# Kernel tuning notes

Measured on AMD Instinct MI355X. Metric: run time of the kernel, lower is better.

## Reference

```python
import jax, jax.numpy as jnp
import numpy as np

N_ATOMS = 10000
N_EDGES = 200000
L_MAX = 2
K_L = [32, 24, 16]  # k_max_l = n_element_channels * n_max_l

# (l1, l2, L) in the original loop order (l1 outer, l2 inner, L ascending)
PAIRS = [(0,0,0),(0,1,1),(0,2,2),
         (1,0,1),(1,1,0),(1,1,1),(1,1,2),(1,2,1),(1,2,2),
         (2,0,2),(2,1,1),(2,1,2),(2,2,0),(2,2,1),(2,2,2)]
# concatenated input width -> k_max_l[L] per (L, sigma) channel
LIN = {'0_1': (72, 32), '1_1': (80, 24), '1_m1': (40, 24), '2_1': (72, 16), '2_m1': (32, 16)}


def setup_inputs() -> dict:
    key = jax.random.key(0)
    it = iter(jax.random.split(key, 64))
    def nrm(shape):
        return jax.random.normal(next(it), shape, dtype=jnp.float32)
    inp = {}
    for l in range(L_MAX + 1):
        inp['rb%d' % l] = nrm((N_EDGES, K_L[l]))           # radial basis per l
    for l in range(L_MAX + 1):
        inp['sh%d' % l] = nrm((N_EDGES, 2*l+1, 1))         # spherical harmonics per l
    inp['emb'] = nrm((N_ATOMS, 1, K_L[0]))                 # initial center embedding
    for l in range(L_MAX + 1):
        inp['f%d' % l] = nrm((N_ATOMS, 2*l+1, K_L[l]))     # nu=1 equivariant features
    for (l1, l2, L) in PAIRS:
        inp['cg_%d_%d_%d' % (l1, l2, L)] = nrm(((2*l1+1)*(2*l2+1), 2*L+1))
    for LS, (fin, fout) in LIN.items():
        inp['W_' + LS] = nrm((fin, fout)) / np.float32(np.sqrt(fin))
        inp['b_' + LS] = nrm((fout,)) * 0.01
    inp['centers'] = jax.random.randint(next(it), (N_EDGES,), 0, N_ATOMS)
    inp['neighbors'] = jax.random.randint(next(it), (N_EDGES,), 0, N_ATOMS)
    inp['n_atoms'] = N_ATOMS
    return inp


def _normalize(x, dims):
    # Normalizer(dims): RMS normalization over the given dims
    return x * jax.lax.rsqrt(jnp.mean(x * x, axis=dims, keepdims=True) + 1e-12)


def _forward(floats, centers, neighbors, n_atoms):
    (rb0, rb1, rb2, sh0, sh1, sh2, emb, f0, f1, f2,
     cg_0_0_0, cg_0_1_1, cg_0_2_2, cg_1_0_1, cg_1_1_0, cg_1_1_1, cg_1_1_2,
     cg_1_2_1, cg_1_2_2, cg_2_0_2, cg_2_1_1, cg_2_1_2, cg_2_2_0, cg_2_2_1,
     cg_2_2_2, W_0_1, b_0_1, W_1_1, b_1_1, W_1_m1, b_1_m1, W_2_1, b_2_1,
     W_2_m1, b_2_m1) = floats
    rb = [rb0, rb1, rb2]; sh = [sh0, sh1, sh2]; feats = [f0, f1, f2]
    cgs = {'0_0_0': cg_0_0_0, '0_1_1': cg_0_1_1, '0_2_2': cg_0_2_2,
           '1_0_1': cg_1_0_1, '1_1_0': cg_1_1_0, '1_1_1': cg_1_1_1,
           '1_1_2': cg_1_1_2, '1_2_1': cg_1_2_1, '1_2_2': cg_1_2_2,
           '2_0_2': cg_2_0_2, '2_1_1': cg_2_1_1, '2_1_2': cg_2_1_2,
           '2_2_0': cg_2_2_0, '2_2_1': cg_2_2_1, '2_2_2': cg_2_2_2}
    lin = {'0_1': (W_0_1, b_0_1), '1_1': (W_1_1, b_1_1), '1_m1': (W_1_m1, b_1_m1),
           '2_1': (W_2_1, b_2_1), '2_m1': (W_2_m1, b_2_m1)}

    # ---- InvariantMessagePasser: density_l = scatter_add over centers of
    #      sh_l * rb_l * emb[neighbors]
    emb_n = emb[neighbors]                                       # [E, 1, k0]
    densities = []
    for l in range(L_MAX + 1):
        msg = sh[l] * rb[l][:, None, :] * emb_n[:, :, :K_L[l]]   # [E, 2l+1, k_l]
        densities.append(jax.ops.segment_sum(msg, centers, num_segments=n_atoms))

    # ---- EquivariantMessagePasser
    ve = [sh[l] * rb[l][:, None, :] for l in range(L_MAX + 1)]   # vector expansion [E,2l+1,k_l]
    fn = [feats[l][neighbors] for l in range(L_MAX + 1)]         # gathered neighbor feats
    results = {}
    for (l1, l2, L) in PAIRS:
        S = (-1) ** (l1 + l2 + L)
        k = min(K_L[l1], K_L[l2])
        t1 = ve[l1][:, :, :k]                                    # [E, 2l1+1, k]
        t2 = fn[l2][:, :, :k]                                    # [E, 2l2+1, k]
        cg = cgs['%d_%d_%d' % (l1, l2, L)].reshape(2*l1+1, 2*l2+1, 2*L+1)
        # fused outer product + CG contraction -> [E, 2L+1, k]
        res = jnp.einsum('eak,ebk,abM->eMk', t1, t2, cg)
        pooled = jax.ops.segment_sum(res, centers, num_segments=n_atoms)
        LS = '%d_%s' % (L, 'm1' if S < 0 else '1')
        results.setdefault(LS, []).append(pooled)

    outs = {}
    for LS, (W, b) in lin.items():
        x = jnp.concatenate(results[LS], axis=2)                 # [n_atoms, 2L+1, size_LS]
        x = _normalize(x, (0, 1))
        x = jnp.einsum('amf,fk->amk', x, W) + b
        outs[LS] = _normalize(x, (0, 1, 2))

    return (densities[0], densities[1], densities[2],
            outs['0_1'], outs['1_1'], outs['1_m1'], outs['2_1'], outs['2_m1'])


def reference(rb0, rb1, rb2, sh0, sh1, sh2, emb, f0, f1, f2,
              cg_0_0_0, cg_0_1_1, cg_0_2_2, cg_1_0_1, cg_1_1_0, cg_1_1_1,
              cg_1_1_2, cg_1_2_1, cg_1_2_2, cg_2_0_2, cg_2_1_1, cg_2_1_2,
              cg_2_2_0, cg_2_2_1, cg_2_2_2, W_0_1, b_0_1, W_1_1, b_1_1,
              W_1_m1, b_1_m1, W_2_1, b_2_1, W_2_m1, b_2_m1,
              centers, neighbors, n_atoms):
    floats = (rb0, rb1, rb2, sh0, sh1, sh2, emb, f0, f1, f2,
              cg_0_0_0, cg_0_1_1, cg_0_2_2, cg_1_0_1, cg_1_1_0, cg_1_1_1,
              cg_1_1_2, cg_1_2_1, cg_1_2_2, cg_2_0_2, cg_2_1_1, cg_2_1_2,
              cg_2_2_0, cg_2_2_1, cg_2_2_2, W_0_1, b_0_1, W_1_1, b_1_1,
              W_1_m1, b_1_m1, W_2_1, b_2_1, W_2_m1, b_2_m1)
    return _forward(floats, centers, neighbors, n_atoms)
```

## Files before the change

kernel.cpp:

```cpp
#include <hip/hip_runtime.h>
#include <hip/hip_bf16.h>

typedef __hip_bfloat16 bf16;

#define N_ATOMS 10000
#define N_EDGES 200000

#define SCG   0
#define SINV  616
#define SS1P  1024
#define SS2P  19968
#define SWS2  20288
#define SINTS 20352
#define IFLAG  0
#define ICOUNT 16
#define IOFFS  10016
#define ICURS  20032
#define IELIST 30032
#define INTS_END_SMALL 230032
#define INTS_END_BIG   430032
#define SXACC (SINTS + INTS_END_BIG)
#define BIG_FLOATS (SXACC + 952*N_ATOMS)

#define O0 0
#define O1 320000
#define O2 1040000
#define OY 1840000

__device__ __forceinline__ float b2f(bf16 x){ return __bfloat162float(x); }
__device__ __forceinline__ bf16  f2b(float x){ return __float2bfloat16(x); }

__device__ __forceinline__ float ldv(const float* p, int i){ return p[i]; }
__device__ __forceinline__ float ldv(const bf16*  p, int i){ return b2f(p[i]); }
__device__ __forceinline__ void  stv(float* p, int i, float v){ p[i] = v; }
__device__ __forceinline__ void  stv(bf16*  p, int i, float v){ p[i] = f2b(v); }

template<typename T> __device__ __forceinline__ int dtid();
// ... 85 lines not shown
    elist[offs[c] + p] = e;
  }
}

__global__ void k_scatter2(const int* __restrict__ centers, const int* __restrict__ neighbors,
                           const int* __restrict__ offs, int* __restrict__ cursors,
                           int2* __restrict__ elist2) {
  int e = blockIdx.x*blockDim.x + threadIdx.x;
  if (e < N_EDGES) {
    int c = centers[e];
    int p = atomicAdd(&cursors[c], 1);
    elist2[offs[c] + p] = make_int2(e, neighbors[e]);
  }
}

template<typename T, int MODE>
__global__ __launch_bounds__(256) void k_main(
    const T* __restrict__ rb0, const T* __restrict__ rb1, const T* __restrict__ rb2,
    const T* __restrict__ sh0, const T* __restrict__ sh1, const T* __restrict__ sh2,
    const T* __restrict__ emb, const T* __restrict__ f0, const T* __restrict__ f1,
    const T* __restrict__ f2, const int* __restrict__ neighbors,
    const int* __restrict__ offs, const int* __restrict__ elist,
    const float* __restrict__ cgf, float* __restrict__ s1p,
    const float* __restrict__ inv, float* __restrict__ s2p,
    float* __restrict__ xout, LinP lp, T* __restrict__ out,
    const int* __restrict__ flag)
{
  if (flag[0] != dtid<T>()) return;
  int lane = threadIdx.x & 63;
  int wv   = threadIdx.x >> 6;
  int a = blockIdx.x;
  int beg = offs[a];
  int cnt = offs[a+1] - beg;
  int k32 = lane & 31, e2 = lane >> 5;
  int k16 = lane & 15, e4 = lane >> 4;
  const int2* el2 = (const int2*)elist;
  int ab = a & 63;

  __shared__ float L[952];
  __shared__ float red[4][5];

  float acc[20];
  #pragma unroll
  for (int i = 0; i < 20; ++i) acc[i] = 0.f;

  if (wv == 0) {
    const float* C000 = cgf + 0;
    const float* C011 = cgf + 1;
    const float* C101 = cgf + 35;
    const float* C110 = cgf + 44;
    const float* C111 = cgf + 53;
    const float* C112 = cgf + 80;
    for (int base = 0; base < cnt; base += 2) {
      int idx = base + e2;
      if (idx < cnt) {
        int e, n;
        if constexpr (MODE == 0) { int2 en = el2[beg + idx]; e = en.x; n = en.y; }
        else { e = elist[beg + idx]; n = neighbors[e]; }
        float s0 = ldv(sh0, e);
        float s1a0 = ldv(sh1, e*3+0), s1a1 = ldv(sh1, e*3+1), s1a2 = ldv(sh1, e*3+2);
        float rb0k = ldv(rb0, e*32 + k32);
        float ek   = ldv(emb, n*32 + k32);
        float f0k  = ldv(f0,  n*32 + k32);
        float ve0 = s0 * rb0k;
        acc[0] = fmaf(ve0, ek, acc[0]);
        acc[4] = fmaf(C000[0]*ve0, f0k, acc[4]);
        if (k32 < 24) {
          float rb1k = ldv(rb1, e*24 + k32);
          float f1k0 = ldv(f1, n*72 + k32);
          float f1k1 = ldv(f1, n*72 + 24 + k32);
          float f1k2 = ldv(f1, n*72 + 48 + k32);
          float rbek = rb1k * ek;
          acc[1] = fmaf(s1a0, rbek, acc[1]);
// ... 29 lines not shown
              for (int M = 0; M < 5; ++M) acc[15+M] = fmaf(p, C112[q*5+M], acc[15+M]);
            }
          }
        }
      }
    }
    #pragma unroll
    for (int i = 0; i < 20; ++i) acc[i] += __shfl_xor(acc[i], 32);
  } else if (wv == 1) {
    const float* C022 = cgf + 10;
    const float* C121 = cgf + 125;
    const float* C122 = cgf + 170;
    for (int base = 0; base < cnt; base += 4) {
      int idx = base + e4;
      if (idx < cnt) {
        int e, n;
        if constexpr (MODE == 0) { int2 en = el2[beg + idx]; e = en.x; n = en.y; }
        else { e = elist[beg + idx]; n = neighbors[e]; }
        float s0 = ldv(sh0, e);
        float s1a[3];
        #pragma unroll
        for (int m = 0; m < 3; ++m) s1a[m] = ldv(sh1, e*3+m);
        float s2a[5];
        #pragma unroll
        for (int m = 0; m < 5; ++m) s2a[m] = ldv(sh2, e*5+m);
        float rb0k = ldv(rb0, e*32 + k16);
        float rb1k = ldv(rb1, e*24 + k16);
        float rb2k = ldv(rb2, e*16 + k16);
        float ek   = ldv(emb, n*32 + k16);
        float f2k[5];
        #pragma unroll
        for (int b = 0; b < 5; ++b) f2k[b] = ldv(f2, n*80 + b*16 + k16);
        float re = rb2k * ek;
// ... 21 lines not shown
        }
      }
    }
    #pragma unroll
    for (int i = 0; i < 18; ++i) {
      acc[i] += __shfl_xor(acc[i], 16);
      acc[i] += __shfl_xor(acc[i], 32);
    }
  } else if (wv == 2) {
    const float* C202 = cgf + 245;
    const float* C211 = cgf + 270;
    const float* C212 = cgf + 315;
    for (int base = 0; base < cnt; base += 4) {
      int idx = base + e4;
      if (idx < cnt) {
        int e, n;
        if constexpr (MODE == 0) { int2 en = el2[beg + idx]; e = en.x; n = en.y; }
        else { e = elist[beg + idx]; n = neighbors[e]; }
        float s2a[5];
        #pragma unroll
        for (int m = 0; m < 5; ++m) s2a[m] = ldv(sh2, e*5+m);
        float rb2k = ldv(rb2, e*16 + k16);
        float f0k  = ldv(f0,  n*32 + k16);
        float f1k[3];
        #pragma unroll
        for (int b = 0; b < 3; ++b) f1k[b] = ldv(f1, n*72 + b*24 + k16);
        float g9 = rb2k * f0k;
        #pragma unroll
        for (int aa = 0; aa < 5; ++aa) {
          float p = g9 * s2a[aa];
          #pragma unroll
          for (int M = 0; M < 5; ++M) acc[0+M] = fmaf(p, C202[aa*5+M], acc[0+M]);
        }
// ... 12 lines not shown
        }
      }
    }
    #pragma unroll
    for (int i = 0; i < 13; ++i) {
      acc[i] += __shfl_xor(acc[i], 16);
      acc[i] += __shfl_xor(acc[i], 32);
    }
  } else {
    const float* C220 = cgf + 390;
    const float* C221 = cgf + 415;
    const float* C222 = cgf + 490;
    for (int base = 0; base < cnt; base += 4) {
      int idx = base + e4;
      if (idx < cnt) {
        int e, n;
        if constexpr (MODE == 0) { int2 en = el2[beg + idx]; e = en.x; n = en.y; }
        else { e = elist[beg + idx]; n = neighbors[e]; }
        float s2a[5];
        #pragma unroll
        for (int m = 0; m < 5; ++m) s2a[m] = ldv(sh2, e*5+m);
        float rb2k = ldv(rb2, e*16 + k16);
        float f2k[5];
        #pragma unroll
        for (int b = 0; b < 5; ++b) f2k[b] = ldv(f2, n*80 + b*16 + k16);
        #pragma unroll
        for (int aa = 0; aa < 5; ++aa) {
          float sa = rb2k * s2a[aa];
          #pragma unroll
          for (int bb = 0; bb < 5; ++bb) {
            float p = sa * f2k[bb];
            int q = aa*5+bb;
            acc[0] = fmaf(p, C220[q], acc[0]);
            #pragma unroll
            for (int M = 0; M < 3; ++M) acc[1+M] = fmaf(p, C221[q*3+M], acc[1+M]);
            #pragma unroll
            for (int M = 0; M < 5; ++M) acc[4+M] = fmaf(p, C222[q*5+M], acc[4+M]);
          }
        }
      }
    }
    #pragma unroll
    for (int i = 0; i < 9; ++i) {
      acc[i] += __shfl_xor(acc[i], 16);
      acc[i] += __shfl_xor(acc[i], 32);
    }
  }

  if constexpr (MODE != 2) {
    if (wv == 0) {
      if (lane < 32) {
        stv(out, O0 + a*32 + k32, acc[0]);
        atomicAdd(&s1p[(0+k32)*64+ab], acc[4]*acc[4]);
        if (k32 < 24) {
          #pragma unroll
          for (int m = 0; m < 3; ++m) stv(out, O1 + a*72 + m*24 + k32, acc[1+m]);
          atomicAdd(&s1p[(32+k32)*64+ab], acc[11]*acc[11]);
          float q;
          q = acc[5]*acc[5]+acc[6]*acc[6]+acc[7]*acc[7];
          atomicAdd(&s1p[(72+k32)*64+ab], q);
          q = acc[8]*acc[8]+acc[9]*acc[9]+acc[10]*acc[10];
          atomicAdd(&s1p[(96+k32)*64+ab], q);
          q = acc[12]*acc[12]+acc[13]*acc[13]+acc[14]*acc[14];
          atomicAdd(&s1p[(152+k32)*64+ab], q);
          q = acc[15]*acc[15]+acc[16]*acc[16]+acc[17]*acc[17]
            + acc[18]*acc[18]+acc[19]*acc[19];
          atomicAdd(&s1p[(208+k32)*64+ab], q);
        }
      }
    } else if (wv == 1) {
      if (lane < 16) {
        #pragma unroll
        for (int m = 0; m < 5; ++m) stv(out, O2 + a*80 + m*16 + k16, acc[m]);
        float q;
        q = acc[5]*acc[5]+acc[6]*acc[6]+acc[7]*acc[7]+acc[8]*acc[8]+acc[9]*acc[9];
        atomicAdd(&s1p[(192+k16)*64+ab], q);
        q = acc[10]*acc[10]+acc[11]*acc[11]+acc[12]*acc[12];
        atomicAdd(&s1p[(120+k16)*64+ab], q);
        q = acc[13]*acc[13]+acc[14]*acc[14]+acc[15]*acc[15]
          + acc[16]*acc[16]+acc[17]*acc[17];
        atomicAdd(&s1p[(264+k16)*64+ab], q);
      }
    } else if (wv == 2) {
      if (lane < 16) {
        float q;
        q = acc[0]*acc[0]+acc[1]*acc[1]+acc[2]*acc[2]+acc[3]*acc[3]+acc[4]*acc[4];
        atomicAdd(&s1p[(232+k16)*64+ab], q);
        q = acc[5]*acc[5]+acc[6]*acc[6]+acc[7]*acc[7];
        atomicAdd(&s1p[(136+k16)*64+ab], q);
        q = acc[8]*acc[8]+acc[9]*acc[9]+acc[10]*acc[10]
          + acc[11]*acc[11]+acc[12]*acc[12];
        atomicAdd(&s1p[(280+k16)*64+ab], q);
      }
    } else {
      if (lane < 16) {
        atomicAdd(&s1p[(56+k16)*64+ab], acc[0]*acc[0]);
        float q;
        q = acc[1]*acc[1]+acc[2]*acc[2]+acc[3]*acc[3];
        atomicAdd(&s1p[(176+k16)*64+ab], q);
        q = acc[4]*acc[4]+acc[5]*acc[5]+acc[6]*acc[6]
          + acc[7]*acc[7]+acc[8]*acc[8];
        atomicAdd(&s1p[(248+k16)*64+ab], q);
      }
    }
  }

  if constexpr (MODE == 0) {
    float* xg = xout + a*952;
    if (wv == 0) {
      if (lane < 32) {
        xg[k32] = acc[4];
        if (k32 < 24) {
          xg[32+k32] = acc[11];
          #pragma unroll
          for (int M = 0; M < 3; ++M) xg[72+M*80+k32]     = acc[5+M];
          #pragma unroll
          for (int M = 0; M < 3; ++M) xg[72+M*80+24+k32]  = acc[8+M];
          #pragma unroll
          for (int M = 0; M < 3; ++M) xg[312+M*40+k32]    = acc[12+M];
          #pragma unroll
          for (int M = 0; M < 5; ++M) xg[432+M*72+16+k32] = acc[15+M];
        }
      }
    } else if (wv == 1) {
      if (lane < 16) {
        #pragma unroll
        for (int M = 0; M < 5; ++M) xg[432+M*72+k16]    = acc[5+M];
        #pragma unroll
        for (int M = 0; M < 3; ++M) xg[72+M*80+48+k16]  = acc[10+M];
        #pragma unroll
        for (int M = 0; M < 5; ++M) xg[792+M*32+k16]    = acc[13+M];
      }
    } else if (wv == 2) {
      if (lane < 16) {
        #pragma unroll
        for (int M = 0; M < 5; ++M) xg[432+M*72+40+k16] = acc[0+M];
        #pragma unroll
        for (int M = 0; M < 3; ++M) xg[72+M*80+64+k16]  = acc[5+M];
        #pragma unroll
        for (int M = 0; M < 5; ++M) xg[792+M*32+16+k16] = acc[8+M];
      }
    } else {
      if (lane < 16) {
        xg[56+k16] = acc[0];
        #pragma unroll
        for (int M = 0; M < 3; ++M) xg[312+M*40+24+k16] = acc[1+M];
        #pragma unroll
        for (int M = 0; M < 5; ++M) xg[432+M*72+56+k16] = acc[4+M];
      }
    }
  }

  if constexpr (MODE == 2) {
    if (wv == 0) {
      if (lane < 32) {
        L[k32] = acc[4]*inv[k32];
        if (k32 < 24) {
          L[32+k32] = acc[11]*inv[32+k32];
          #pragma unroll
          for (int M = 0; M < 3; ++M) L[72+M*80+k32]     = acc[5+M]*inv[72+k32];
          #pragma unroll
          for (int M = 0; M < 3; ++M) L[72+M*80+24+k32]  = acc[8+M]*inv[96+k32];
          #pragma unroll
          for (int M = 0; M < 3; ++M) L[312+M*40+k32]    = acc[12+M]*inv[152+k32];
          #pragma unroll
          for (int M = 0; M < 5; ++M) L[432+M*72+16+k32] = acc[15+M]*inv[208+k32];
        }
      }
    } else if (wv == 1) {
      if (lane < 16) {
        #pragma unroll
        for (int M = 0; M < 5; ++M) L[432+M*72+k16]    = acc[5+M]*inv[192+k16];
        #pragma unroll
        for (int M = 0; M < 3; ++M) L[72+M*80+48+k16]  = acc[10+M]*inv[120+k16];
        #pragma unroll
        for (int M = 0; M < 5; ++M) L[792+M*32+k16]    = acc[13+M]*inv[264+k16];
      }
    } else if (wv == 2) {
      if (lane < 16) {
        #pragma unroll
        for (int M = 0; M < 5; ++M) L[432+M*72+40+k16] = acc[0+M]*inv[232+k16];
        #pragma unroll
        for (int M = 0; M < 3; ++M) L[72+M*80+64+k16]  = acc[5+M]*inv[136+k16];
        #pragma unroll
        for (int M = 0; M < 5; ++M) L[792+M*32+16+k16] = acc[8+M]*inv[280+k16];
      }
    } else {
      if (lane < 16) {
        L[56+k16] = acc[0]*inv[56+k16];
        #pragma unroll
        for (int M = 0; M < 3; ++M) L[312+M*40+24+k16] = acc[1+M]*inv[176+k16];
        #pragma unroll
        for (int M = 0; M < 5; ++M) L[432+M*72+56+k16] = acc[4+M]*inv[248+k16];
      }
    }
    __syncthreads();
    int t = threadIdx.x;
    float y2[5] = {0.f,0.f,0.f,0.f,0.f};
    for (int tau = t; tau < 336; tau += 256) {
      int ls = 0;
      while (tau >= c_cum[ls+1]) ++ls;
      int rem = tau - c_cum[ls];
      int kn = c_kout[ls], fin = c_fin[ls];
      int M = rem / kn, ko = rem - M*kn;
      const T* W = (const T*)lp.W[ls];
      float y = ldv((const T*)lp.B[ls], ko);
      const float* xv = &L[c_xb[ls] + M*fin];
      for (int f = 0; f < fin; ++f) y = fmaf(xv[f], ldv(W, f*kn+ko), y);
      stv(out, c_yoff[ls] + (a*c_Ms[ls] + M)*kn + ko, y);
      y2[ls] += y*y;
    }
    #pragma unroll
    for (int i = 0; i < 5; ++i) {
      y2[i] += __shfl_xor(y2[i], 1);  y2[i] += __shfl_xor(y2[i], 2);
      y2[i] += __shfl_xor(y2[i], 4);  y2[i] += __shfl_xor(y2[i], 8);
      y2[i] += __shfl_xor(y2[i], 16); y2[i] += __shfl_xor(y2[i], 32);
    }
    if (lane == 0) {
      #pragma unroll
      for (int i = 0; i < 5; ++i) red[wv][i] = y2[i];
    }
    __syncthreads();
    if (t == 0) {
      #pragma unroll
      for (int i = 0; i < 5; ++i)
        atomicAdd(&s2p[i*64 + ab], red[0][i]+red[1][i]+red[2][i]+red[3][i]);
    }
  }
}

template<typename T>
__global__ __launch_bounds__(256) void k_lin(
    const float* __restrict__ xg, const float* __restrict__ inv,
    LinP lp, T* __restrict__ out, float* __restrict__ s2p,
    const int* __restrict__ flag)
{
  if (flag[0] != dtid<T>()) return;
  int a = blockIdx.x;
  int t = threadIdx.x;
  __shared__ float L[952];
  for (int i = t; i < 952; i += 256) {
    int ch;
    if      (i < 72)  ch = i;
    else if (i < 312) ch = 72  + (i-72)  % 80;
    else if (i < 432) ch = 152 + (i-312) % 40;
    else if (i < 792) ch = 192 + (i-432) % 72;
    else              ch = 264 + (i-792) % 32;
    L[i] = xg[a*952 + i] * inv[ch];
  }
  __syncthreads();
  float y2[5] = {0.f,0.f,0.f,0.f,0.f};
  for (int tau = t; tau < 336; tau += 256) {
    int ls = 0;
    while (tau >= c_cum[ls+1]) ++ls;
    int rem = tau - c_cum[ls];
    int kn = c_kout[ls], fin = c_fin[ls];
    int M = rem / kn, ko = rem - M*kn;
    const T* W = (const T*)lp.W[ls];
    float y = ldv((const T*)lp.B[ls], ko);
    const float* xv = &L[c_xb[ls] + M*fin];
    for (int f = 0; f < fin; ++f) y = fmaf(xv[f], ldv(W, f*kn+ko), y);
    stv(out, c_yoff[ls] + (a*c_Ms[ls] + M)*kn + ko, y);
    y2[ls] += y*y;
// ... 37 lines not shown
}

template<typename T>
__global__ void k_scale(const float* __restrict__ ws2, T* __restrict__ out,
                        const int* __restrict__ flag) {
  if (flag[0] != dtid<T>()) return;
  int i = blockIdx.x*blockDim.x + threadIdx.x;
  if (i >= 3360000) return;
  int ls = (i < 320000) ? 0 : (i < 1040000) ? 1 : (i < 1760000) ? 2 : (i < 2560000) ? 3 : 4;
  float scale = rsqrtf(ws2[ls] / (float)c_numel[ls] + 1e-12f);
  stv(out, OY + i, ldv((const T*)out, OY + i) * scale);
}

template<typename T>
static void launch_chain(void* const* d_in, T* out, float* wsf, int* wsi,
                         Ptrs15 cg, LinP lp, bool big, hipStream_t stream) {
  const T* rb0 = (const T*)d_in[0];
  const T* rb1 = (const T*)d_in[1];
  const T* rb2 = (const T*)d_in[2];
  const T* sh0 = (const T*)d_in[3];
  const T* sh1 = (const T*)d_in[4];
  const T* sh2 = (const T*)d_in[5];
  const T* emb = (const T*)d_in[6];
  const T* f0  = (const T*)d_in[7];
  const T* f1  = (const T*)d_in[8];
  const T* f2  = (const T*)d_in[9];
  const int* neighbors = (const int*)d_in[36];
  const int* flag = wsi + IFLAG;

  k_cg<T><<<3, 256, 0, stream>>>(cg, wsf, flag);
  if (big) {
    k_main<T,0><<<N_ATOMS, 256, 0, stream>>>(rb0, rb1, rb2, sh0, sh1, sh2, emb, f0, f1, f2,
        neighbors, wsi+IOFFS, wsi+IELIST, wsf+SCG, wsf+SS1P, nullptr, nullptr,
        wsf+SXACC, lp, out, flag);
    k_red1<<<296, 64, 0, stream>>>(wsf+SS1P, wsf+SINV);
    k_lin<T><<<N_ATOMS, 256, 0, stream>>>(wsf+SXACC, wsf+SINV, lp, out, wsf+SS2P, flag);
  } else {
    k_main<T,1><<<N_ATOMS, 256, 0, stream>>>(rb0, rb1, rb2, sh0, sh1, sh2, emb, f0, f1, f2,
        neighbors, wsi+IOFFS, wsi+IELIST, wsf+SCG, wsf+SS1P, nullptr, nullptr,
        nullptr, lp, out, flag);
    k_red1<<<296, 64, 0, stream>>>(wsf+SS1P, wsf+SINV);
    k_main<T,2><<<N_ATOMS, 256, 0, stream>>>(rb0, rb1, rb2, sh0, sh1, sh2, emb, f0, f1, f2,
        neighbors, wsi+IOFFS, wsi+IELIST, wsf+SCG, nullptr, wsf+SINV, wsf+SS2P,
        nullptr, lp, out, flag);
  }
  k_red2<<<5, 64, 0, stream>>>(wsf+SS2P, wsf+SWS2);
  k_scale<T><<<(3360000+255)/256, 256, 0, stream>>>(wsf+SWS2, out, flag);
}

extern "C" void kernel_launch(void* const* d_in, const int* in_sizes, int n_in,
                              void* d_out, int out_size, void* d_ws, size_t ws_size,
                              hipStream_t stream) {
  float* wsf = (float*)d_ws;
  int*   wsi = (int*)(wsf + SINTS);
  const int* centers   = (const int*)d_in[35];
  const int* neighbors = (const int*)d_in[36];
  bool big = ws_size >= (size_t)BIG_FLOATS * 4;

  Ptrs15 cg;
  for (int i = 0; i < 15; ++i) cg.p[i] = d_in[10+i];
  LinP lp;
  lp.W[0] = d_in[25]; lp.B[0] = d_in[26];
  lp.W[1] = d_in[27]; lp.B[1] = d_in[28];
  lp.W[2] = d_in[29]; lp.B[2] = d_in[30];
  lp.W[3] = d_in[31]; lp.B[3] = d_in[32];
  lp.W[4] = d_in[33]; lp.B[4] = d_in[34];

  k_probe<<<1, 64, 0, stream>>>((const unsigned short*)d_in[0],
                                (const unsigned short*)d_in[6], wsi + IFLAG);
  k_zero<<<154, 256, 0, stream>>>(wsf, wsi);
  k_hist<<<(N_EDGES+255)/256, 256, 0, stream>>>(centers, wsi+ICOUNT);
  k_scan<<<1, 1024, 0, stream>>>(wsi+ICOUNT, wsi+IOFFS);
  if (big) {
    k_scatter2<<<(N_EDGES+255)/256, 256, 0, stream>>>(centers, neighbors, wsi+IOFFS,
                                                      wsi+ICURS, (int2*)(wsi+IELIST));
  } else {
    k_scatter<<<(N_EDGES+255)/256, 256, 0, stream>>>(centers, wsi+IOFFS, wsi+ICURS, wsi+IELIST);
  }

  launch_chain<bf16 >(d_in, (bf16*)d_out,  wsf, wsi, cg, lp, big, stream);
  launch_chain<float>(d_in, (float*)d_out, wsf, wsi, cg, lp, big, stream);
}
```

Measured before the change: 516.4 us.

## Split per-atom edge kernel into 13 balanced single-wave work groups

Replaces the 4-wave-per-atom main kernel, whose waves carried very unequal numbers of CG products, with a kernel that launches 13 single-wave blocks per atom. Each block handles a smaller, more even subset of the tensor-product outputs. The pre-linear intermediate buffer is now stored in bf16 instead of fp32, which cuts its write and read traffic. In exchange, neighbor features and edge data are re-gathered by several groups per atom, and the intermediate loses precision.

```diff
diff --git a/kernel.cpp b/kernel.cpp
--- a/kernel.cpp
+++ b/kernel.cpp
@@ -5,6 +5,7 @@
 
 #define N_ATOMS 10000
 #define N_EDGES 200000
+#define NGRP 13
 
 #define SCG   0
 #define SINV  616
@@ -19,8 +20,8 @@
 #define IELIST 30032
 #define INTS_END_SMALL 230032
 #define INTS_END_BIG   430032
-#define SXACC (SINTS + INTS_END_BIG)
-#define BIG_FLOATS (SXACC + 952*N_ATOMS)
+#define XBF_BYTE_OFF ((size_t)SINTS*4 + (size_t)INTS_END_BIG*4)
+#define BIG_BYTES (XBF_BYTE_OFF + (size_t)952*N_ATOMS*2)
 
 #define O0 0
 #define O1 320000
@@ -136,16 +137,381 @@
   }
 }
 
-template<typename T, int MODE>
-__global__ __launch_bounds__(256) void k_main(
+template<typename T, int BIGX>
+__global__ __launch_bounds__(64) void k_grp(
     const T* __restrict__ rb0, const T* __restrict__ rb1, const T* __restrict__ rb2,
     const T* __restrict__ sh0, const T* __restrict__ sh1, const T* __restrict__ sh2,
     const T* __restrict__ emb, const T* __restrict__ f0, const T* __restrict__ f1,
     const T* __restrict__ f2, const int* __restrict__ neighbors,
     const int* __restrict__ offs, const int* __restrict__ elist,
     const float* __restrict__ cgf, float* __restrict__ s1p,
-    const float* __restrict__ inv, float* __restrict__ s2p,
-    float* __restrict__ xout, LinP lp, T* __restrict__ out,
+    bf16* __restrict__ xout, T* __restrict__ out, const int* __restrict__ flag)
+{
+  if (flag[0] != dtid<T>()) return;
+  int bx = blockIdx.x;
+  int g = bx % NGRP, a = bx / NGRP;
+  int lane = threadIdx.x;
+  int beg = offs[a];
+  int cnt = offs[a+1] - beg;
+  int k32 = lane & 31, e2 = lane >> 5;
+  int k16 = lane & 15, e4 = lane >> 4;
+  int ab = a & 63;
+  const int2* el2 = (const int2*)elist;
+  bf16* xg = xout + a*952;
+
+#define FETCH_EN(idx) int e, n; \
+    if constexpr (BIGX) { int2 en = el2[beg + (idx)]; e = en.x; n = en.y; } \
+    else { e = elist[beg + (idx)]; n = neighbors[e]; }
+
+  if (g == 0) {
+    const float* C011 = cgf + 1;
+    const float* C101 = cgf + 35;
+    const float* C110 = cgf + 44;
+    float C000v = cgf[0];
+    float acc[12];
+    #pragma unroll
+    for (int i = 0; i < 12; ++i) acc[i] = 0.f;
+    for (int base = 0; base < cnt; base += 2) {
+      int idx = base + e2;
+      if (idx < cnt) {
+        FETCH_EN(idx)
+        float s0 = ldv(sh0, e);
+        float s1a0 = ldv(sh1, e*3+0), s1a1 = ldv(sh1, e*3+1), s1a2 = ldv(sh1, e*3+2);
+        float rb0k = ldv(rb0, e*32 + k32);
+        float ek   = ldv(emb, n*32 + k32);
+        float f0k  = ldv(f0,  n*32 + k32);
+        float ve0 = s0 * rb0k;
+        acc[0] = fmaf(ve0, ek, acc[0]);
+        acc[4] = fmaf(C000v*ve0, f0k, acc[4]);
+        if (k32 < 24) {
+          float rb1k = ldv(rb1, e*24 + k32);
+          float f1k0 = ldv(f1, n*72 + k32);
+          float f1k1 = ldv(f1, n*72 + 24 + k32);
+          float f1k2 = ldv(f1, n*72 + 48 + k32);
+          float rbek = rb1k * ek;
+          acc[1] = fmaf(s1a0, rbek, acc[1]);
+          acc[2] = fmaf(s1a1, rbek, acc[2]);
+          acc[3] = fmaf(s1a2, rbek, acc[3]);
+          #pragma unroll
+          for (int bb = 0; bb < 3; ++bb) {
+            float fb = (bb==0)?f1k0:(bb==1)?f1k1:f1k2;
+            float p = ve0 * fb;
+            #pragma unroll
+            for (int M = 0; M < 3; ++M) acc[5+M] = fmaf(p, C011[bb*3+M], acc[5+M]);
+          }
+          float gv = rb1k * f0k;
+          #pragma unroll
+          for (int aa = 0; aa < 3; ++aa) {
+            float sa = (aa==0)?s1a0:(aa==1)?s1a1:s1a2;
+            float p = gv * sa;
+            #pragma unroll
+            for (int M = 0; M < 3; ++M) acc[8+M] = fmaf(p, C101[aa*3+M], acc[8+M]);
+          }
+          #pragma unroll
+          for (int aa = 0; aa < 3; ++aa) {
+            float sa = rb1k * ((aa==0)?s1a0:(aa==1)?s1a1:s1a2);
+            #pragma unroll
+            for (int bb = 0; bb < 3; ++bb) {
+              float fb = (bb==0)?f1k0:(bb==1)?f1k1:f1k2;
+              acc[11] = fmaf(sa*fb, C110[aa*3+bb], acc[11]);
+            }
+          }
+        }
+      }
+    }
+    #pragma unroll
+    for (int i = 0; i < 12; ++i) acc[i] += __shfl_xor(acc[i], 32);
+    if (lane < 32) {
+      stv(out, O0 + a*32 + k32, acc[0]);
+      atomicAdd(&s1p[(0+k32)*64+ab], acc[4]*acc[4]);
+      if (BIGX) xg[k32] = f2b(acc[4]);
+      if (k32 < 24) {
+        #pragma unroll
+        for (int m = 0; m < 3; ++m) stv(out, O1 + a*72 + m*24 + k32, acc[1+m]);
+        atomicAdd(&s1p[(32+k32)*64+ab], acc[11]*acc[11]);
+        atomicAdd(&s1p[(72+k32)*64+ab], acc[5]*acc[5]+acc[6]*acc[6]+acc[7]*acc[7]);
+        atomicAdd(&s1p[(96+k32)*64+ab], acc[8]*acc[8]+acc[9]*acc[9]+acc[10]*acc[10]);
+        if (BIGX) {
+          xg[32+k32] = f2b(acc[11]);
+          #pragma unroll
+          for (int M = 0; M < 3; ++M) xg[72+M*80+k32]    = f2b(acc[5+M]);
+          #pragma unroll
+          for (int M = 0; M < 3; ++M) xg[72+M*80+24+k32] = f2b(acc[8+M]);
+        }
+      }
+    }
+  } else if (g == 1 || g == 2) {
+    const float* C = (g == 1) ? (cgf + 53) : (cgf + 80);
+    const int NM = (g == 1) ? 3 : 5;
+    float acc[5] = {0.f,0.f,0.f,0.f,0.f};
+    for (int base = 0; base < cnt; base += 2) {
+      int idx = base + e2;
+      if (idx < cnt && k32 < 24) {
+        FETCH_EN(idx)
+        float s1a0 = ldv(sh1, e*3+0), s1a1 = ldv(sh1, e*3+1), s1a2 = ldv(sh1, e*3+2);
+        float rb1k = ldv(rb1, e*24 + k32);
+        float f1k0 = ldv(f1, n*72 + k32);
+        float f1k1 = ldv(f1, n*72 + 24 + k32);
+        float f1k2 = ldv(f1, n*72 + 48 + k32);
+        #pragma unroll
+        for (int aa = 0; aa < 3; ++aa) {
+          float sa = rb1k * ((aa==0)?s1a0:(aa==1)?s1a1:s1a2);
+          #pragma unroll
+          for (int bb = 0; bb < 3; ++bb) {
+            float fb = (bb==0)?f1k0:(bb==1)?f1k1:f1k2;
+            float p = sa * fb;
+            int q = aa*3+bb;
+            for (int M = 0; M < NM; ++M) acc[M] = fmaf(p, C[q*NM+M], acc[M]);
+          }
+        }
+      }
+    }
+    #pragma unroll
+    for (int i = 0; i < 5; ++i) acc[i] += __shfl_xor(acc[i], 32);
+    if (lane < 24) {
+      float q2 = 0.f;
+      for (int M = 0; M < NM; ++M) q2 += acc[M]*acc[M];
+      int ch = (g == 1) ? (152+k32) : (208+k32);
+      atomicAdd(&s1p[ch*64+ab], q2);
+      if (BIGX) {
+        if (g == 1) { for (int M = 0; M < 3; ++M) xg[312+M*40+k32]    = f2b(acc[M]); }
+        else        { for (int M = 0; M < 5; ++M) xg[432+M*72+16+k32] = f2b(acc[M]); }
+      }
+    }
+  } else if (g == 3) {
+    const float* C022 = cgf + 10;
+    float acc[10];
+    #pragma unroll
+    for (int i = 0; i < 10; ++i) acc[i] = 0.f;
+    for (int base = 0; base < cnt; base += 4) {
+      int idx = base + e4;
+      if (idx < cnt) {
+        FETCH_EN(idx)
+        float s2a[5];
+        #pragma unroll
+        for (int m = 0; m < 5; ++m) s2a[m] = ldv(sh2, e*5+m);
+        float rb2k = ldv(rb2, e*16 + k16);
+        float ek   = ldv(emb, n*32 + k16);
+        float re = rb2k * ek;
+        #pragma unroll
+        for (int m = 0; m < 5; ++m) acc[m] = fmaf(s2a[m], re, acc[m]);
+        float s0 = ldv(sh0, e);
+        float rb0k = ldv(rb0, e*32 + k16);
+        float ve0 = s0 * rb0k;
+        #pragma unroll
+        for (int bb = 0; bb < 5; ++bb) {
+          float p = ve0 * ldv(f2, n*80 + bb*16 + k16);
+          #pragma unroll
+          for (int M = 0; M < 5; ++M) acc[5+M] = fmaf(p, C022[bb*5+M], acc[5+M]);
+        }
+      }
+    }
+    #pragma unroll
+    for (int i = 0; i < 10; ++i) {
+      acc[i] += __shfl_xor(acc[i], 16);
+      acc[i] += __shfl_xor(acc[i], 32);
+    }
+    if (lane < 16) {
+      #pragma unroll
+      for (int m = 0; m < 5; ++m) stv(out, O2 + a*80 + m*16 + k16, acc[m]);
+      atomicAdd(&s1p[(192+k16)*64+ab],
+                acc[5]*acc[5]+acc[6]*acc[6]+acc[7]*acc[7]+acc[8]*acc[8]+acc[9]*acc[9]);
+      if (BIGX) { for (int M = 0; M < 5; ++M) xg[432+M*72+k16] = f2b(acc[5+M]); }
+    }
+  } else if (g == 4 || g == 5) {
+    const float* C = (g == 4) ? (cgf + 125) : (cgf + 170);
+    const int NM = (g == 4) ? 3 : 5;
+    float acc[5] = {0.f,0.f,0.f,0.f,0.f};
+    for (int base = 0; base < cnt; base += 4) {
+      int idx = base + e4;
+      if (idx < cnt) {
+        FETCH_EN(idx)
+        float s1a[3];
+        #pragma unroll
+        for (int m = 0; m < 3; ++m) s1a[m] = ldv(sh1, e*3+m);
+        float rb1k = ldv(rb1, e*24 + k16);
+        float f2k[5];
+        #pragma unroll
+        for (int b = 0; b < 5; ++b) f2k[b] = ldv(f2, n*80 + b*16 + k16);
+        #pragma unroll
+        for (int aa = 0; aa < 3; ++aa) {
+          float sa = rb1k * s1a[aa];
+          #pragma unroll
+          for (int bb = 0; bb < 5; ++bb) {
+            float p = sa * f2k[bb];
+            int q = aa*5+bb;
+            for (int M = 0; M < NM; ++M) acc[M] = fmaf(p, C[q*NM+M], acc[M]);
+          }
+        }
+      }
+    }
+    #pragma unroll
+    for (int i = 0; i < 5; ++i) {
+      acc[i] += __shfl_xor(acc[i], 16);
+      acc[i] += __shfl_xor(acc[i], 32);
+    }
+    if (lane < 16) {
+      float q2 = 0.f;
+      for (int M = 0; M < NM; ++M) q2 += acc[M]*acc[M];
+      int ch = (g == 4) ? (120+k16) : (264+k16);
+      atomicAdd(&s1p[ch*64+ab], q2);
+      if (BIGX) {
+        if (g == 4) { for (int M = 0; M < 3; ++M) xg[72+M*80+48+k16] = f2b(acc[M]); }
+        else        { for (int M = 0; M < 5; ++M) xg[792+M*32+k16]   = f2b(acc[M]); }
+      }
+    }
+  } else if (g == 6) {
+    const float* C202 = cgf + 245;
+    float acc[5] = {0.f,0.f,0.f,0.f,0.f};
+    for (int base = 0; base < cnt; base += 4) {
+      int idx = base + e4;
+      if (idx < cnt) {
+        FETCH_EN(idx)
+        float s2a[5];
+        #pragma unroll
+        for (int m = 0; m < 5; ++m) s2a[m] = ldv(sh2, e*5+m);
+        float rb2k = ldv(rb2, e*16 + k16);
+        float f0k  = ldv(f0,  n*32 + k16);
+        float gv = rb2k * f0k;
+        #pragma unroll
+        for (int aa = 0; aa < 5; ++aa) {
+          float p = gv * s2a[aa];
+          #pragma unroll
+          for (int M = 0; M < 5; ++M) acc[M] = fmaf(p, C202[aa*5+M], acc[M]);
+        }
+      }
+    }
+    #pragma unroll
+    for (int i = 0; i < 5; ++i) {
+      acc[i] += __shfl_xor(acc[i], 16);
+      acc[i] += __shfl_xor(acc[i], 32);
+    }
+    if (lane < 16) {
+      atomicAdd(&s1p[(232+k16)*64+ab],
+                acc[0]*acc[0]+acc[1]*acc[1]+acc[2]*acc[2]+acc[3]*acc[3]+acc[4]*acc[4]);
+      if (BIGX) { for (int M = 0; M < 5; ++M) xg[432+M*72+40+k16] = f2b(acc[M]); }
+    }
+  } else if (g == 7 || g == 8) {
+    const float* C = (g == 7) ? (cgf + 270) : (cgf + 315);
+    const int NM = (g == 7) ? 3 : 5;
+    float acc[5] = {0.f,0.f,0.f,0.f,0.f};
+    for (int base = 0; base < cnt; base += 4) {
+      int idx = base + e4;
+      if (idx < cnt) {
+        FETCH_EN(idx)
+        float s2a[5];
+        #pragma unroll
+        for (int m = 0; m < 5; ++m) s2a[m] = ldv(sh2, e*5+m);
+        float rb2k = ldv(rb2, e*16 + k16);
+        float f1k[3];
+        #pragma unroll
+        for (int b = 0; b < 3; ++b) f1k[b] = ldv(f1, n*72 + b*24 + k16);
+        #pragma unroll
+        for (int aa = 0; aa < 5; ++aa) {
+          float sa = rb2k * s2a[aa];
+          #pragma unroll
+          for (int bb = 0; bb < 3; ++bb) {
+            float p = sa * f1k[bb];
+            int q = aa*3+bb;
+            for (int M = 0; M < NM; ++M) acc[M] = fmaf(p, C[q*NM+M], acc[M]);
+          }
+        }
+      }
+    }
+    #pragma unroll
+    for (int i = 0; i < 5; ++i) {
+      acc[i] += __shfl_xor(acc[i], 16);
+      acc[i] += __shfl_xor(acc[i], 32);
+    }
+    if (lane < 16) {
+      float q2 = 0.f;
+      for (int M = 0; M < NM; ++M) q2 += acc[M]*acc[M];
+      int ch = (g == 7) ? (136+k16) : (280+k16);
+      atomicAdd(&s1p[ch*64+ab], q2);
+      if (BIGX) {
+        if (g == 7) { for (int M = 0; M < 3; ++M) xg[72+M*80+64+k16]  = f2b(acc[M]); }
+        else        { for (int M = 0; M < 5; ++M) xg[792+M*32+16+k16] = f2b(acc[M]); }
+      }
+    }
+  } else {
+    const float* C220 = cgf + 390;
+    const float* C221 = cgf + 415;
+    const float* C222 = cgf + 490;
+    float acc[3] = {0.f,0.f,0.f};
+    for (int base = 0; base < cnt; base += 4) {
+      int idx = base + e4;
+      if (idx < cnt) {
+        FETCH_EN(idx)
+        float s2a[5];
+        #pragma unroll
+        for (int m = 0; m < 5; ++m) s2a[m] = ldv(sh2, e*5+m);
+        float rb2k = ldv(rb2, e*16 + k16);
+        float f2k[5];
+        #pragma unroll
+        for (int b = 0; b < 5; ++b) f2k[b] = ldv(f2, n*80 + b*16 + k16);
+        #pragma unroll
+        for (int aa = 0; aa < 5; ++aa) {
+          float sa = rb2k * s2a[aa];
+          #pragma unroll
+          for (int bb = 0; bb < 5; ++bb) {
+            float p = sa * f2k[bb];
+            int q = aa*5+bb;
+            if (g == 9) {
+              acc[0] = fmaf(p, C220[q],     acc[0]);
+              acc[1] = fmaf(p, C221[q*3],   acc[1]);
+            } else if (g == 10) {
+              acc[0] = fmaf(p, C221[q*3+1], acc[0]);
+              acc[1] = fmaf(p, C221[q*3+2], acc[1]);
+            } else if (g == 11) {
+              acc[0] = fmaf(p, C222[q*5],   acc[0]);
+              acc[1] = fmaf(p, C222[q*5+1], acc[1]);
+            } else {
+              acc[0] = fmaf(p, C222[q*5+2], acc[0]);
+              acc[1] = fmaf(p, C222[q*5+3], acc[1]);
+              acc[2] = fmaf(p, C222[q*5+4], acc[2]);
+            }
+          }
+        }
+      }
+    }
+    #pragma unroll
+    for (int i = 0; i < 3; ++i) {
+      acc[i] += __shfl_xor(acc[i], 16);
+      acc[i] += __shfl_xor(acc[i], 32);
+    }
+    if (lane < 16) {
+      if (g == 9) {
+        atomicAdd(&s1p[(56+k16)*64+ab],  acc[0]*acc[0]);
+        atomicAdd(&s1p[(176+k16)*64+ab], acc[1]*acc[1]);
+        if (BIGX) { xg[56+k16] = f2b(acc[0]); xg[312+24+k16] = f2b(acc[1]); }
+      } else if (g == 10) {
+        atomicAdd(&s1p[(176+k16)*64+ab], acc[0]*acc[0]+acc[1]*acc[1]);
+        if (BIGX) { xg[312+40+24+k16] = f2b(acc[0]); xg[312+80+24+k16] = f2b(acc[1]); }
+      } else if (g == 11) {
+        atomicAdd(&s1p[(248+k16)*64+ab], acc[0]*acc[0]+acc[1]*acc[1]);
+        if (BIGX) { xg[432+56+k16] = f2b(acc[0]); xg[432+72+56+k16] = f2b(acc[1]); }
+      } else {
+        atomicAdd(&s1p[(248+k16)*64+ab],
+                  acc[0]*acc[0]+acc[1]*acc[1]+acc[2]*acc[2]);
+        if (BIGX) {
+          #pragma unroll
+          for (int j = 0; j < 3; ++j) xg[432+(2+j)*72+56+k16] = f2b(acc[j]);
+        }
+      }
+    }
+  }
+#undef FETCH_EN
+}
+
+template<typename T>
+__global__ __launch_bounds__(256) void k_pass2(
+    const T* __restrict__ rb0, const T* __restrict__ rb1, const T* __restrict__ rb2,
+    const T* __restrict__ sh0, const T* __restrict__ sh1, const T* __restrict__ sh2,
+    const T* __restrict__ emb, const T* __restrict__ f0, const T* __restrict__ f1,
+    const T* __restrict__ f2, const int* __restrict__ neighbors,
+    const int* __restrict__ offs, const int* __restrict__ elist,
+    const float* __restrict__ cgf, const float* __restrict__ inv,
+    float* __restrict__ s2p, LinP lp, T* __restrict__ out,
     const int* __restrict__ flag)
 {
   if (flag[0] != dtid<T>()) return;
@@ -156,7 +522,6 @@
   int cnt = offs[a+1] - beg;
   int k32 = lane & 31, e2 = lane >> 5;
   int k16 = lane & 15, e4 = lane >> 4;
-  const int2* el2 = (const int2*)elist;
   int ab = a & 63;
 
   __shared__ float L[952];
@@ -176,9 +541,8 @@
     for (int base = 0; base < cnt; base += 2) {
       int idx = base + e2;
       if (idx < cnt) {
-        int e, n;
-        if constexpr (MODE == 0) { int2 en = el2[beg + idx]; e = en.x; n = en.y; }
-        else { e = elist[beg + idx]; n = neighbors[e]; }
+        int e = elist[beg + idx];
+        int n = neighbors[e];
         float s0 = ldv(sh0, e);
         float s1a0 = ldv(sh1, e*3+0), s1a1 = ldv(sh1, e*3+1), s1a2 = ldv(sh1, e*3+2);
         float rb0k = ldv(rb0, e*32 + k32);
@@ -238,9 +602,8 @@
     for (int base = 0; base < cnt; base += 4) {
       int idx = base + e4;
       if (idx < cnt) {
-        int e, n;
-        if constexpr (MODE == 0) { int2 en = el2[beg + idx]; e = en.x; n = en.y; }
-        else { e = elist[beg + idx]; n = neighbors[e]; }
+        int e = elist[beg + idx];
+        int n = neighbors[e];
         float s0 = ldv(sh0, e);
         float s1a[3];
         #pragma unroll
@@ -292,9 +655,8 @@
     for (int base = 0; base < cnt; base += 4) {
       int idx = base + e4;
       if (idx < cnt) {
-        int e, n;
-        if constexpr (MODE == 0) { int2 en = el2[beg + idx]; e = en.x; n = en.y; }
-        else { e = elist[beg + idx]; n = neighbors[e]; }
+        int e = elist[beg + idx];
+        int n = neighbors[e];
         float s2a[5];
         #pragma unroll
         for (int m = 0; m < 5; ++m) s2a[m] = ldv(sh2, e*5+m);
@@ -337,9 +699,8 @@
     for (int base = 0; base < cnt; base += 4) {
       int idx = base + e4;
       if (idx < cnt) {
-        int e, n;
-        if constexpr (MODE == 0) { int2 en = el2[beg + idx]; e = en.x; n = en.y; }
-        else { e = elist[beg + idx]; n = neighbors[e]; }
+        int e = elist[beg + idx];
+        int n = neighbors[e];
         float s2a[5];
         #pragma unroll
         for (int m = 0; m < 5; ++m) s2a[m] = ldv(sh2, e*5+m);
@@ -370,191 +731,85 @@
     }
   }
 
-  if constexpr (MODE != 2) {
-    if (wv == 0) {
-      if (lane < 32) {
-        stv(out, O0 + a*32 + k32, acc[0]);
-        atomicAdd(&s1p[(0+k32)*64+ab], acc[4]*acc[4]);
-        if (k32 < 24) {
-          #pragma unroll
-          for (int m = 0; m < 3; ++m) stv(out, O1 + a*72 + m*24 + k32, acc[1+m]);
-          atomicAdd(&s1p[(32+k32)*64+ab], acc[11]*acc[11]);
-          float q;
-          q = acc[5]*acc[5]+acc[6]*acc[6]+acc[7]*acc[7];
-          atomicAdd(&s1p[(72+k32)*64+ab], q);
-          q = acc[8]*acc[8]+acc[9]*acc[9]+acc[10]*acc[10];
-          atomicAdd(&s1p[(96+k32)*64+ab], q);
-          q = acc[12]*acc[12]+acc[13]*acc[13]+acc[14]*acc[14];
-          atomicAdd(&s1p[(152+k32)*64+ab], q);
-          q = acc[15]*acc[15]+acc[16]*acc[16]+acc[17]*acc[17]
-            + acc[18]*acc[18]+acc[19]*acc[19];
-          atomicAdd(&s1p[(208+k32)*64+ab], q);
-        }
-      }
-    } else if (wv == 1) {
-      if (lane < 16) {
-        #pragma unroll
-        for (int m = 0; m < 5; ++m) stv(out, O2 + a*80 + m*16 + k16, acc[m]);
-        float q;
-        q = acc[5]*acc[5]+acc[6]*acc[6]+acc[7]*acc[7]+acc[8]*acc[8]+acc[9]*acc[9];
-        atomicAdd(&s1p[(192+k16)*64+ab], q);
-        q = acc[10]*acc[10]+acc[11]*acc[11]+acc[12]*acc[12];
-        atomicAdd(&s1p[(120+k16)*64+ab], q);
-        q = acc[13]*acc[13]+acc[14]*acc[14]+acc[15]*acc[15]
-          + acc[16]*acc[16]+acc[17]*acc[17];
-        atomicAdd(&s1p[(264+k16)*64+ab], q);
-      }
-    } else if (wv == 2) {
-      if (lane < 16) {
-        float q;
-        q = acc[0]*acc[0]+acc[1]*acc[1]+acc[2]*acc[2]+acc[3]*acc[3]+acc[4]*acc[4];
-        atomicAdd(&s1p[(232+k16)*64+ab], q);
-        q = acc[5]*acc[5]+acc[6]*acc[6]+acc[7]*acc[7];
-        atomicAdd(&s1p[(136+k16)*64+ab], q);
-        q = acc[8]*acc[8]+acc[9]*acc[9]+acc[10]*acc[10]
-          + acc[11]*acc[11]+acc[12]*acc[12];
-        atomicAdd(&s1p[(280+k16)*64+ab], q);
-      }
-    } else {
-      if (lane < 16) {
-        atomicAdd(&s1p[(56+k16)*64+ab], acc[0]*acc[0]);
-        float q;
-        q = acc[1]*acc[1]+acc[2]*acc[2]+acc[3]*acc[3];
-        atomicAdd(&s1p[(176+k16)*64+ab], q);
-        q = acc[4]*acc[4]+acc[5]*acc[5]+acc[6]*acc[6]
-          + acc[7]*acc[7]+acc[8]*acc[8];
-        atomicAdd(&s1p[(248+k16)*64+ab], q);
-      }
-    }
-  }
-
-  if constexpr (MODE == 0) {
-    float* xg = xout + a*952;
-    if (wv == 0) {
-      if (lane < 32) {
-        xg[k32] = acc[4];
-        if (k32 < 24) {
-          xg[32+k32] = acc[11];
-          #pragma unroll
-          for (int M = 0; M < 3; ++M) xg[72+M*80+k32]     = acc[5+M];
-          #pragma unroll
-          for (int M = 0; M < 3; ++M) xg[72+M*80+24+k32]  = acc[8+M];
-          #pragma unroll
-          for (int M = 0; M < 3; ++M) xg[312+M*40+k32]    = acc[12+M];
-          #pragma unroll
-          for (int M = 0; M < 5; ++M) xg[432+M*72+16+k32] = acc[15+M];
-        }
-      }
-    } else if (wv == 1) {
-      if (lane < 16) {
-        #pragma unroll
-        for (int M = 0; M < 5; ++M) xg[432+M*72+k16]    = acc[5+M];
-        #pragma unroll
-        for (int M = 0; M < 3; ++M) xg[72+M*80+48+k16]  = acc[10+M];
-        #pragma unroll
-        for (int M = 0; M < 5; ++M) xg[792+M*32+k16]    = acc[13+M];
-      }
-    } else if (wv == 2) {
-      if (lane < 16) {
-        #pragma unroll
-        for (int M = 0; M < 5; ++M) xg[432+M*72+40+k16] = acc[0+M];
-        #pragma unroll
-        for (int M = 0; M < 3; ++M) xg[72+M*80+64+k16]  = acc[5+M];
-        #pragma unroll
-        for (int M = 0; M < 5; ++M) xg[792+M*32+16+k16] = acc[8+M];
-      }
-    } else {
-      if (lane < 16) {
-        xg[56+k16] = acc[0];
-        #pragma unroll
-        for (int M = 0; M < 3; ++M) xg[312+M*40+24+k16] = acc[1+M];
-        #pragma unroll
-        for (int M = 0; M < 5; ++M) xg[432+M*72+56+k16] = acc[4+M];
-      }
-    }
-  }
-
-  if constexpr (MODE == 2) {
-    if (wv == 0) {
-      if (lane < 32) {
-        L[k32] = acc[4]*inv[k32];
-        if (k32 < 24) {
-          L[32+k32] = acc[11]*inv[32+k32];
-          #pragma unroll
-          for (int M = 0; M < 3; ++M) L[72+M*80+k32]     = acc[5+M]*inv[72+k32];
-          #pragma unroll
-          for (int M = 0; M < 3; ++M) L[72+M*80+24+k32]  = acc[8+M]*inv[96+k32];
-          #pragma unroll
-          for (int M = 0; M < 3; ++M) L[312+M*40+k32]    = acc[12+M]*inv[152+k32];
-          #pragma unroll
-          for (int M = 0; M < 5; ++M) L[432+M*72+16+k32] = acc[15+M]*inv[208+k32];
-        }
-      }
-    } else if (wv == 1) {
-      if (lane < 16) {
-        #pragma unroll
-        for (int M = 0; M < 5; ++M) L[432+M*72+k16]    = acc[5+M]*inv[192+k16];
-        #pragma unroll
-        for (int M = 0; M < 3; ++M) L[72+M*80+48+k16]  = acc[10+M]*inv[120+k16];
-        #pragma unroll
-        for (int M = 0; M < 5; ++M) L[792+M*32+k16]    = acc[13+M]*inv[264+k16];
-      }
-    } else if (wv == 2) {
-      if (lane < 16) {
-        #pragma unroll
-        for (int M = 0; M < 5; ++M) L[432+M*72+40+k16] = acc[0+M]*inv[232+k16];
-        #pragma unroll
-        for (int M = 0; M < 3; ++M) L[72+M*80+64+k16]  = acc[5+M]*inv[136+k16];
-        #pragma unroll
-        for (int M = 0; M < 5; ++M) L[792+M*32+16+k16] = acc[8+M]*inv[280+k16];
-      }
-    } else {
-      if (lane < 16) {
-        L[56+k16] = acc[0]*inv[56+k16];
-        #pragma unroll
-        for (int M = 0; M < 3; ++M) L[312+M*40+24+k16] = acc[1+M]*inv[176+k16];
-        #pragma unroll
-        for (int M = 0; M < 5; ++M) L[432+M*72+56+k16] = acc[4+M]*inv[248+k16];
-      }
-    }
-    __syncthreads();
-    int t = threadIdx.x;
-    float y2[5] = {0.f,0.f,0.f,0.f,0.f};
-    for (int tau = t; tau < 336; tau += 256) {
-      int ls = 0;
-      while (tau >= c_cum[ls+1]) ++ls;
-      int rem = tau - c_cum[ls];
-      int kn = c_kout[ls], fin = c_fin[ls];
-      int M = rem / kn, ko = rem - M*kn;
-      const T* W = (const T*)lp.W[ls];
-      float y = ldv((const T*)lp.B[ls], ko);
-      const float* xv = &L[c_xb[ls] + M*fin];
-      for (int f = 0; f < fin; ++f) y = fmaf(xv[f], ldv(W, f*kn+ko), y);
-      stv(out, c_yoff[ls] + (a*c_Ms[ls] + M)*kn + ko, y);
-      y2[ls] += y*y;
-    }
-    #pragma unroll
-    for (int i = 0; i < 5; ++i) {
-      y2[i] += __shfl_xor(y2[i], 1);  y2[i] += __shfl_xor(y2[i], 2);
-      y2[i] += __shfl_xor(y2[i], 4);  y2[i] += __shfl_xor(y2[i], 8);
-      y2[i] += __shfl_xor(y2[i], 16); y2[i] += __shfl_xor(y2[i], 32);
-    }
-    if (lane == 0) {
+  if (wv == 0) {
+    if (lane < 32) {
+      L[k32] = acc[4]*inv[k32];
+      if (k32 < 24) {
+        L[32+k32] = acc[11]*inv[32+k32];
+        #pragma unroll
+        for (int M = 0; M < 3; ++M) L[72+M*80+k32]     = acc[5+M]*inv[72+k32];
+        #pragma unroll
+        for (int M = 0; M < 3; ++M) L[72+M*80+24+k32]  = acc[8+M]*inv[96+k32];
+        #pragma unroll
+        for (int M = 0; M < 3; ++M) L[312+M*40+k32]    = acc[12+M]*inv[152+k32];
+        #pragma unroll
+        for (int M = 0; M < 5; ++M) L[432+M*72+16+k32] = acc[15+M]*inv[208+k32];
+      }
+    }
+  } else if (wv == 1) {
+    if (lane < 16) {
       #pragma unroll
-      for (int i = 0; i < 5; ++i) red[wv][i] = y2[i];
-    }
-    __syncthreads();
-    if (t == 0) {
+      for (int M = 0; M < 5; ++M) L[432+M*72+k16]    = acc[5+M]*inv[192+k16];
       #pragma unroll
-      for (int i = 0; i < 5; ++i)
-        atomicAdd(&s2p[i*64 + ab], red[0][i]+red[1][i]+red[2][i]+red[3][i]);
-    }
+      for (int M = 0; M < 3; ++M) L[72+M*80+48+k16]  = acc[10+M]*inv[120+k16];
+      #pragma unroll
+      for (int M = 0; M < 5; ++M) L[792+M*32+k16]    = acc[13+M]*inv[264+k16];
+    }
+  } else if (wv == 2) {
+    if (lane < 16) {
+      #pragma unroll
+      for (int M = 0; M < 5; ++M) L[432+M*72+40+k16] = acc[0+M]*inv[232+k16];
+      #pragma unroll
+      for (int M = 0; M < 3; ++M) L[72+M*80+64+k16]  = acc[5+M]*inv[136+k16];
+      #pragma unroll
+      for (int M = 0; M < 5; ++M) L[792+M*32+16+k16] = acc[8+M]*inv[280+k16];
+    }
+  } else {
+    if (lane < 16) {
+      L[56+k16] = acc[0]*inv[56+k16];
+      #pragma unroll
+      for (int M = 0; M < 3; ++M) L[312+M*40+24+k16] = acc[1+M]*inv[176+k16];
+      #pragma unroll
+      for (int M = 0; M < 5; ++M) L[432+M*72+56+k16] = acc[4+M]*inv[248+k16];
+    }
+  }
+  __syncthreads();
+  int t = threadIdx.x;
+  float y2[5] = {0.f,0.f,0.f,0.f,0.f};
+  for (int tau = t; tau < 336; tau += 256) {
+    int ls = 0;
+    while (tau >= c_cum[ls+1]) ++ls;
+    int rem = tau - c_cum[ls];
+    int kn = c_kout[ls], fin = c_fin[ls];
+    int M = rem / kn, ko = rem - M*kn;
+    const T* W = (const T*)lp.W[ls];
+    float y = ldv((const T*)lp.B[ls], ko);
+    const float* xv = &L[c_xb[ls] + M*fin];
+    for (int f = 0; f < fin; ++f) y = fmaf(xv[f], ldv(W, f*kn+ko), y);
+    stv(out, c_yoff[ls] + (a*c_Ms[ls] + M)*kn + ko, y);
+    y2[ls] += y*y;
+  }
+  #pragma unroll
+  for (int i = 0; i < 5; ++i) {
+    y2[i] += __shfl_xor(y2[i], 1);  y2[i] += __shfl_xor(y2[i], 2);
+    y2[i] += __shfl_xor(y2[i], 4);  y2[i] += __shfl_xor(y2[i], 8);
+    y2[i] += __shfl_xor(y2[i], 16); y2[i] += __shfl_xor(y2[i], 32);
+  }
+  if (lane == 0) {
+    #pragma unroll
+    for (int i = 0; i < 5; ++i) red[wv][i] = y2[i];
+  }
+  __syncthreads();
+  if (t == 0) {
+    #pragma unroll
+    for (int i = 0; i < 5; ++i)
+      atomicAdd(&s2p[i*64 + ab], red[0][i]+red[1][i]+red[2][i]+red[3][i]);
   }
 }
 
 template<typename T>
 __global__ __launch_bounds__(256) void k_lin(
-    const float* __restrict__ xg, const float* __restrict__ inv,
+    const bf16* __restrict__ xg, const float* __restrict__ inv,
     LinP lp, T* __restrict__ out, float* __restrict__ s2p,
     const int* __restrict__ flag)
 {
@@ -569,7 +824,7 @@
     else if (i < 432) ch = 152 + (i-312) % 40;
     else if (i < 792) ch = 192 + (i-432) % 72;
     else              ch = 264 + (i-792) % 32;
-    L[i] = xg[a*952 + i] * inv[ch];
+    L[i] = b2f(xg[a*952 + i]) * inv[ch];
   }
   __syncthreads();
   float y2[5] = {0.f,0.f,0.f,0.f,0.f};
@@ -637,7 +892,8 @@
 
 template<typename T>
 static void launch_chain(void* const* d_in, T* out, float* wsf, int* wsi,
-                         Ptrs15 cg, LinP lp, bool big, hipStream_t stream) {
+                         bf16* xbf, Ptrs15 cg, LinP lp, bool big,
+                         hipStream_t stream) {
   const T* rb0 = (const T*)d_in[0];
   const T* rb1 = (const T*)d_in[1];
   const T* rb2 = (const T*)d_in[2];
@@ -653,19 +909,19 @@
 
   k_cg<T><<<3, 256, 0, stream>>>(cg, wsf, flag);
   if (big) {
-    k_main<T,0><<<N_ATOMS, 256, 0, stream>>>(rb0, rb1, rb2, sh0, sh1, sh2, emb, f0, f1, f2,
-        neighbors, wsi+IOFFS, wsi+IELIST, wsf+SCG, wsf+SS1P, nullptr, nullptr,
-        wsf+SXACC, lp, out, flag);
+    k_grp<T,1><<<N_ATOMS*NGRP, 64, 0, stream>>>(rb0, rb1, rb2, sh0, sh1, sh2, emb,
+        f0, f1, f2, neighbors, wsi+IOFFS, wsi+IELIST, wsf+SCG, wsf+SS1P,
+        xbf, out, flag);
     k_red1<<<296, 64, 0, stream>>>(wsf+SS1P, wsf+SINV);
-    k_lin<T><<<N_ATOMS, 256, 0, stream>>>(wsf+SXACC, wsf+SINV, lp, out, wsf+SS2P, flag);
+    k_lin<T><<<N_ATOMS, 256, 0, stream>>>(xbf, wsf+SINV, lp, out, wsf+SS2P, flag);
   } else {
-    k_main<T,1><<<N_ATOMS, 256, 0, stream>>>(rb0, rb1, rb2, sh0, sh1, sh2, emb, f0, f1, f2,
-        neighbors, wsi+IOFFS, wsi+IELIST, wsf+SCG, wsf+SS1P, nullptr, nullptr,
-        nullptr, lp, out, flag);
+    k_grp<T,0><<<N_ATOMS*NGRP, 64, 0, stream>>>(rb0, rb1, rb2, sh0, sh1, sh2, emb,
+        f0, f1, f2, neighbors, wsi+IOFFS, wsi+IELIST, wsf+SCG, wsf+SS1P,
+        nullptr, out, flag);
     k_red1<<<296, 64, 0, stream>>>(wsf+SS1P, wsf+SINV);
-    k_main<T,2><<<N_ATOMS, 256, 0, stream>>>(rb0, rb1, rb2, sh0, sh1, sh2, emb, f0, f1, f2,
-        neighbors, wsi+IOFFS, wsi+IELIST, wsf+SCG, nullptr, wsf+SINV, wsf+SS2P,
-        nullptr, lp, out, flag);
+    k_pass2<T><<<N_ATOMS, 256, 0, stream>>>(rb0, rb1, rb2, sh0, sh1, sh2, emb,
+        f0, f1, f2, neighbors, wsi+IOFFS, wsi+IELIST, wsf+SCG, wsf+SINV,
+        wsf+SS2P, lp, out, flag);
   }
   k_red2<<<5, 64, 0, stream>>>(wsf+SS2P, wsf+SWS2);
   k_scale<T><<<(3360000+255)/256, 256, 0, stream>>>(wsf+SWS2, out, flag);
@@ -676,9 +932,10 @@
                               hipStream_t stream) {
   float* wsf = (float*)d_ws;
   int*   wsi = (int*)(wsf + SINTS);
+  bf16*  xbf = (bf16*)((char*)d_ws + XBF_BYTE_OFF);
   const int* centers   = (const int*)d_in[35];
   const int* neighbors = (const int*)d_in[36];
-  bool big = ws_size >= (size_t)BIG_FLOATS * 4;
+  bool big = ws_size >= BIG_BYTES;
 
   Ptrs15 cg;
   for (int i = 0; i < 15; ++i) cg.p[i] = d_in[10+i];
@@ -701,6 +958,6 @@
     k_scatter<<<(N_EDGES+255)/256, 256, 0, stream>>>(centers, wsi+IOFFS, wsi+ICURS, wsi+IELIST);
   }
 
-  launch_chain<bf16 >(d_in, (bf16*)d_out,  wsf, wsi, cg, lp, big, stream);
-  launch_chain<float>(d_in, (float*)d_out, wsf, wsi, cg, lp, big, stream);
-}
+  launch_chain<bf16 >(d_in, (bf16*)d_out,  wsf, wsi, xbf, cg, lp, big, stream);
+  launch_chain<float>(d_in, (float*)d_out, wsf, wsi, xbf, cg, lp, big, stream);
+}
```

New measurement: 1.087 ms. +110.6%, slower.
